# Optimization experiments

Hardware: AMD Instinct MI355X
Metric: run time of the kernel (lower is better)

Reference implementation:

```python
import jax, jax.numpy as jnp
import numpy as np

H = 16      # num_heads = num_channels // head_dim
D = 128     # head_dim
BLK = 64    # NABLA / flex_attention block size
THR = 0.8   # sparse_params['P'] cumulative-density threshold
EPS = 1e-6  # RMSNorm eps


def _rmsnorm(x, w):
    # torch nn.RMSNorm over last dim (computed in fp32 as in norm_qk)
    return x * jax.lax.rsqrt(jnp.mean(x * x, axis=-1, keepdims=True) + EPS) * w


def _rotate_half(x):
    x1, x2 = jnp.split(x, 2, axis=-1)
    return jnp.concatenate([-x2, x1], axis=-1)


def _apply_rotary(x, cos, sin):
    # x: [S, H, D]; cos/sin: [S, 1, D]
    return x * cos + _rotate_half(x) * sin


def _nabla_block_mask(q, k, sta_mask):
    # q, k: [H, S, D] -> block-pooled attention map, cumulative-density threshold
    Hh, S, Dd = q.shape
    nb = S // BLK
    qb = q.reshape(Hh, nb, BLK, Dd).mean(axis=2)           # [H, nQ, D]
    kb = k.reshape(Hh, nb, BLK, Dd).mean(axis=2)           # [H, nK, D]
    p = jax.nn.softmax(jnp.einsum('hqd,hkd->hqk', qb, kb) / np.sqrt(Dd), axis=-1)
    srt = -jnp.sort(-p, axis=-1)                           # descending
    csum = jnp.cumsum(srt, axis=-1)
    keep_sorted = (csum - srt) < THR                       # smallest set covering THR mass
    cutoff = jnp.min(jnp.where(keep_sorted, srt, jnp.inf), axis=-1, keepdims=True)
    return (p >= cutoff) | sta_mask[None]                  # [H, nQ, nK] bool


def reference(x, rope_cos, rope_sin, sta_mask, Wq, bq, Wk, bk, Wv, bv, Wo, bo, qn_w, kn_w):
    S, C = x.shape
    q = (x @ Wq + bq).reshape(S, H, D)
    k = (x @ Wk + bk).reshape(S, H, D)
    v = (x @ Wv + bv).reshape(S, H, D)
    q = _rmsnorm(q, qn_w)
    k = _rmsnorm(k, kn_w)
    q = _apply_rotary(q, rope_cos, rope_sin)
    k = _apply_rotary(k, rope_cos, rope_sin)
    q = q.transpose(1, 0, 2)  # [H, S, D]
    k = k.transpose(1, 0, 2)
    v = v.transpose(1, 0, 2)
    blk_keep = _nabla_block_mask(q, k, sta_mask)                     # [H, nQ, nK]
    mask = jnp.repeat(jnp.repeat(blk_keep, BLK, axis=1), BLK, axis=2)  # [H, S, S]
    scores = jnp.einsum('hqd,hkd->hqk', q, k) / np.sqrt(D)
    scores = jnp.where(mask, scores, -jnp.inf)
    attn = jax.nn.softmax(scores, axis=-1)
    out = jnp.einsum('hqk,hkd->hqd', attn, v)                        # [H, S, D]
    out = out.transpose(1, 0, 2).reshape(S, H * D)
    return out @ Wo + bo


def setup_inputs() -> dict:
    key = jax.random.key(0)
    ks = jax.random.split(key, 12)
    S, C = 2048, 2048
    nb = S // BLK
    sc = 0.02
    return {
        'x': jax.random.normal(ks[0], (S, C), jnp.float32),
        'rope_cos': jax.random.uniform(ks[1], (S, 1, D), jnp.float32),
        'rope_sin': jax.random.uniform(ks[2], (S, 1, D), jnp.float32),
        'sta_mask': jax.random.randint(ks[3], (nb, nb), 0, 2).astype(bool),
        'Wq': jax.random.normal(ks[4], (C, C), jnp.float32) * sc,
        'bq': jnp.zeros((C,), jnp.float32),
        'Wk': jax.random.normal(ks[5], (C, C), jnp.float32) * sc,
        'bk': jnp.zeros((C,), jnp.float32),
        'Wv': jax.random.normal(ks[6], (C, C), jnp.float32) * sc,
        'bv': jnp.zeros((C,), jnp.float32),
        'Wo': jax.random.normal(ks[7], (C, C), jnp.float32) * sc,
        'bo': jnp.zeros((C,), jnp.float32),
        'qn_w': jnp.ones((D,), jnp.float32),
        'kn_w': jnp.ones((D,), jnp.float32),
    }
```

## Files before the change

### kernel.cpp

```cpp
#include <hip/hip_runtime.h>


#define S_LEN 2048
#define CDIM  2048
#define NH    16
#define HD    128
#define NB    32

typedef __attribute__((ext_vector_type(8))) short s8v;
typedef __attribute__((ext_vector_type(4))) short s4v;
typedef __attribute__((ext_vector_type(4))) float f4v;

__device__ __forceinline__ short f2bf(float f){
  unsigned u = __builtin_bit_cast(unsigned, f);
  u += 0x7fffu + ((u>>16)&1u);
  return (short)(u>>16);
}
__device__ __forceinline__ float bf2f(short s){
  unsigned u = ((unsigned)(unsigned short)s)<<16;
  return __builtin_bit_cast(float, u);
}
__device__ __forceinline__ void gload_lds16(const void* g, void* l){
  __builtin_amdgcn_global_load_lds(
      (const __attribute__((address_space(1))) void*)g,
      (__attribute__((address_space(3))) void*)l, 16, 0, 0);
}

__global__ void __launch_bounds__(256) conv_x_kernel(
    const float* __restrict__ x, short* __restrict__ xcat)
{
  int i = blockIdx.x*256 + threadIdx.x;
  f4v v = ((const f4v*)x)[i];
  int s = i >> 9, c4 = (i & 511)*4;
  s4v hi, lo;
#pragma unroll
  for (int e=0;e<4;e++){
    short h = f2bf(v[e]);
    hi[e] = h;
    lo[e] = f2bf(v[e] - bf2f(h));
  }
  short* row = xcat + (size_t)s*4096 + c4;
  *(s4v*)(row)        = hi;
  *(s4v*)(row + 2048) = lo;
}

__global__ void __launch_bounds__(256) conv_w3_kernel(
    const float* __restrict__ Wq, const float* __restrict__ Wk,
    short* __restrict__ wcat)
{
  __shared__ float tile[64][65];
  const float* W = blockIdx.z ? Wk : Wq;
  short* out = wcat + (size_t)blockIdx.z*2048*4096;
  const int k0 = blockIdx.y*64, n0 = blockIdx.x*64, t = threadIdx.x;
#pragma unroll
  for (int i=0;i<16;i++){
    int idx = i*256 + t, r = idx>>6, c = idx&63;
    tile[r][c] = W[(size_t)(k0+r)*2048 + (n0+c)];
  }
  __syncthreads();
#pragma unroll
  for (int i=0;i<16;i++){
    int idx = i*256 + t, n = idx>>6, k = idx&63;
    float v = tile[k][n];
    short h  = f2bf(v);
    short lo = f2bf(v - bf2f(h));
    short* base = out + (size_t)(n0+n)*4096 + (k0+k);
    base[0]    = h;
    base[2048] = lo;
  }
}

__global__ void __launch_bounds__(256) conv_w1_kernel(
    const float* __restrict__ Wv, const float* __restrict__ Wo,
    short* __restrict__ wtv, short* __restrict__ wto)
{
  __shared__ float tile[64][65];
  const float* W = blockIdx.z ? Wo : Wv;
  short* wt = blockIdx.z ? wto : wtv;
  const int k0 = blockIdx.y*64, n0 = blockIdx.x*64, t = threadIdx.x;
#pragma unroll
  for (int i=0;i<16;i++){
    int idx = i*256 + t, r = idx>>6, c = idx&63;
    tile[r][c] = W[(size_t)(k0+r)*2048 + (n0+c)];
  }
  __syncthreads();
#pragma unroll
  for (int i=0;i<16;i++){
    int idx = i*256 + t, n = idx>>6, k = idx&63;
    wt[(size_t)(n0+n)*2048 + (k0+k)] = f2bf(tile[k][n]);
  }
}

template<int OUT>
__global__ void __launch_bounds__(512, 4) gemm8_bt(
    const short* __restrict__ A, int lda,
    const short* __restrict__ Bt, int ldb,
    const float* __restrict__ biasQ, const float* __restrict__ biasK,
    int nsplit,
    void* __restrict__ Cout, int ldc, int K, int ntiles,
    int awrap, int asub, int bwrap, int bsub)
{
  __shared__ short Alds[2][128*64];
  __shared__ short Blds[2][128*64];
  const int t = threadIdx.x, w = t>>6, l = t&63;
  const int nwg = gridDim.x;
  const int bid = blockIdx.x;
  const int swz = (bid & 7)*(nwg>>3) + (bid>>3);
  const int mi = swz / ntiles, ni = swz % ntiles;
  const int m0 = mi*128, n0 = ni*128;
  const int wr = w>>2, wc = w&3;
  const int l16 = l&15, lg = l>>4;

  f4v acc[4][2];
  f4v z = {0.f,0.f,0.f,0.f};
#pragma unroll
  for (int a=0;a<4;a++)
#pragma unroll
    for (int b=0;b<2;b++) acc[a][b] = z;

  const int srow = w*16 + (l>>3);
  const int scol = ((l&7) ^ ((l>>3)&7)) * 8;
  const short* Ag = A  + (size_t)(m0 + srow)*lda + scol;
  const short* Bg = Bt + (size_t)(n0 + srow)*ldb + scol;

  auto stageAB = [&](int buf, int kt){
    const int ak = kt - ((kt >= awrap) ? asub : 0);
    const int bk2 = kt - ((kt >= bwrap) ? bsub : 0);
#pragma unroll
    for (int ii=0;ii<2;ii++){
      gload_lds16(Ag + (size_t)ii*8*lda + ak, (char*)Alds[buf] + w*2048 + ii*1024);
      gload_lds16(Bg + (size_t)ii*8*ldb + bk2, (char*)Blds[buf] + w*2048 + ii*1024);
    }
  };

  stageAB(0, 0);
  int cur = 0;
  for (int kt = 0; kt < K; kt += 64){
    if (kt + 64 < K){
      stageAB(cur^1, kt+64);
      asm volatile("s_waitcnt vmcnt(4)" ::: "memory");
    } else {
      asm volatile("s_waitcnt vmcnt(0)" ::: "memory");
    }
    __builtin_amdgcn_s_barrier();
    const char* Al = (const char*)Alds[cur];
    const char* Bl = (const char*)Blds[cur];
#pragma unroll
    for (int kk=0;kk<2;kk++){
      const int swx = ((l16&7)<<4);
      s8v af[4], bfv[2];
#pragma unroll
      for (int mt=0;mt<4;mt++)
        af[mt]  = *(const s8v*)(Al + (wr*64+mt*16+l16)*128 + ((kk*64 + lg*16) ^ swx));
#pragma unroll
      for (int jt=0;jt<2;jt++)
        bfv[jt] = *(const s8v*)(Bl + (wc*32+jt*16+l16)*128 + ((kk*64 + lg*16) ^ swx));
      __builtin_amdgcn_s_setprio(1);
#pragma unroll
      for (int mt=0;mt<4;mt++)
#pragma unroll
        for (int jt=0;jt<2;jt++)
          acc[mt][jt] = __builtin_amdgcn_mfma_f32_16x16x32_bf16(
              af[mt], bfv[jt], acc[mt][jt], 0, 0, 0);
      __builtin_amdgcn_s_setprio(0);
    }
    asm volatile("" ::: "memory");
    __builtin_amdgcn_s_barrier();
    cur ^= 1;
  }

  const float* bp = (n0 >= nsplit) ? (biasK + (n0 - nsplit)) : (biasQ + n0);
#pragma unroll
  for (int mt=0;mt<4;mt++)
#pragma unroll
    for (int r=0;r<4;r++){
      int row = m0 + wr*64 + mt*16 + lg*4 + r;
#pragma unroll
      for (int jt=0;jt<2;jt++){
        int cr = wc*32 + jt*16 + l16;
        float v = acc[mt][jt][r] + bp[cr];
        if (OUT == 0) ((float*)Cout)[(size_t)row*ldc + n0 + cr] = v;
        else          ((short*)Cout)[(size_t)row*ldc + n0 + cr] = f2bf(v);
      }
    }
}

template<int OUT>
__global__ void __launch_bounds__(512, 6) gemm8_n64(
    const short* __restrict__ A, int lda,
    const short* __restrict__ Bt, int ldb,
    const float* __restrict__ bias,
    void* __restrict__ Cout, int ldc, int K, int ntiles)
{
  __shared__ short Alds[2][128*64];
  __shared__ short Blds[2][64*64];
  const int t = threadIdx.x, w = t>>6, l = t&63;
  const int nwg = gridDim.x;
  const int bid = blockIdx.x;
  const int swz = (bid & 7)*(nwg>>3) + (bid>>3);
  const int mi = swz / ntiles, ni = swz % ntiles;
  const int m0 = mi*128, n0 = ni*64;
  const int wr = w>>2, wc = w&3;
  const int l16 = l&15, lg = l>>4;

  f4v acc[4];
  f4v z = {0.f,0.f,0.f,0.f};
#pragma unroll
  for (int a=0;a<4;a++) acc[a] = z;

  const int srA = w*16 + (l>>3);
  const int srB = w*8  + (l>>3);
  const int scol = ((l&7) ^ ((l>>3)&7)) * 8;
  const short* Ag = A  + (size_t)(m0 + srA)*lda + scol;
  const short* Bg = Bt + (size_t)(n0 + srB)*ldb + scol;

  auto stageAB = [&](int buf, int kt){
#pragma unroll
    for (int ii=0;ii<2;ii++)
      gload_lds16(Ag + (size_t)ii*8*lda + kt, (char*)Alds[buf] + w*2048 + ii*1024);
    gload_lds16(Bg + kt, (char*)Blds[buf] + w*1024);
  };

  stageAB(0, 0);
  int cur = 0;
  for (int kt = 0; kt < K; kt += 64){
    if (kt + 64 < K){
      stageAB(cur^1, kt+64);
      asm volatile("s_waitcnt vmcnt(3)" ::: "memory");
    } else {
      asm volatile("s_waitcnt vmcnt(0)" ::: "memory");
    }
    __builtin_amdgcn_s_barrier();
    const char* Al = (const char*)Alds[cur];
    const char* Bl = (const char*)Blds[cur];
#pragma unroll
    for (int kk=0;kk<2;kk++){
      const int swx = ((l16&7)<<4);
      s8v af[4], bfv;
#pragma unroll
      for (int mt=0;mt<4;mt++)
        af[mt] = *(const s8v*)(Al + (wr*64+mt*16+l16)*128 + ((kk*64 + lg*16) ^ swx));
      bfv = *(const s8v*)(Bl + (wc*16+l16)*128 + ((kk*64 + lg*16) ^ swx));
      __builtin_amdgcn_s_setprio(1);
#pragma unroll
      for (int mt=0;mt<4;mt++)
        acc[mt] = __builtin_amdgcn_mfma_f32_16x16x32_bf16(af[mt], bfv, acc[mt], 0,0,0);
      __builtin_amdgcn_s_setprio(0);
    }
    asm volatile("" ::: "memory");
    __builtin_amdgcn_s_barrier();
    cur ^= 1;
  }

#pragma unroll
  for (int mt=0;mt<4;mt++)
#pragma unroll
    for (int r=0;r<4;r++){
      int row = m0 + wr*64 + mt*16 + lg*4 + r;
      int cr = wc*16 + l16;
      float v = acc[mt][r] + bias[n0 + cr];
      if (OUT == 0) ((float*)Cout)[(size_t)row*ldc + n0 + cr] = v;
      else          ((short*)Cout)[(size_t)row*ldc + n0 + cr] = f2bf(v);
    }
}

__global__ void __launch_bounds__(256) qk_post_kernel(
    const float* __restrict__ QKf,
    const float* __restrict__ qw, const float* __restrict__ kw,
    const float* __restrict__ rc, const float* __restrict__ rs,
    short* __restrict__ Qh, short* __restrict__ Kh,
    float* __restrict__ Qb, float* __restrict__ Kb)
{
  __shared__ float pool[4][128];
  const int sb = blockIdx.x, h = blockIdx.y, which = blockIdx.z;
  const float* in    = QKf + (which ? 2048 : 0);
  const float* wvp   = which ? kw : qw;
  short*       outp  = which ? Kh : Qh;
  float*       poolp = which ? Kb : Qb;
  const int t = threadIdx.x, w = t>>6, l = t&63;
  const int s = sb*64 + w*16 + (l>>2), d0 = (l&3)*32;

  float a[32];
  const f4v* src = (const f4v*)(in + (size_t)s*4096 + h*128 + d0);
#pragma unroll
  for (int i=0;i<8;i++){
    f4v v = src[i];
    a[i*4]=v[0]; a[i*4+1]=v[1]; a[i*4+2]=v[2]; a[i*4+3]=v[3];
  }
  float ss = 0.f;
#pragma unroll
  for (int i=0;i<32;i++) ss += a[i]*a[i];
  ss += __shfl_xor(ss,1); ss += __shfl_xor(ss,2);
  float rstd = 1.0f / sqrtf(ss*(1.0f/128.0f) + 1e-6f);

  const f4v* wv4 = (const f4v*)(wvp + d0);
#pragma unroll
  for (int i=0;i<8;i++){
    f4v wv = wv4[i];
    a[i*4]   *= rstd*wv[0]; a[i*4+1] *= rstd*wv[1];
    a[i*4+2] *= rstd*wv[2]; a[i*4+3] *= rstd*wv[3];
  }
  float cv[32], sv[32];
  const f4v* cs4 = (const f4v*)(rc + (size_t)s*128 + d0);
  const f4v* sn4 = (const f4v*)(rs + (size_t)s*128 + d0);
#pragma unroll
  for (int i=0;i<8;i++){
    f4v c = cs4[i], sn = sn4[i];
    cv[i*4]=c[0]; cv[i*4+1]=c[1]; cv[i*4+2]=c[2]; cv[i*4+3]=c[3];
    sv[i*4]=sn[0]; sv[i*4+1]=sn[1]; sv[i*4+2]=sn[2]; sv[i*4+3]=sn[3];
  }
  const float sgn = (l&2) ? 1.f : -1.f;
#pragma unroll
  for (int i=0;i<32;i++){
    float pv = __shfl_xor(a[i], 2);
    a[i] = a[i]*cv[i] + sgn*pv*sv[i];
  }
  short* op = outp + ((size_t)h*2048 + s)*128 + d0;
#pragma unroll
  for (int c8=0;c8<8;c8++){
    s4v ob;
#pragma unroll
    for (int e=0;e<4;e++) ob[e] = f2bf(a[c8*4+e]);
    ((s4v*)op)[c8] = ob;
  }
#pragma unroll
  for (int i=0;i<32;i++){
    a[i] += __shfl_xor(a[i],4);
    a[i] += __shfl_xor(a[i],8);
    a[i] += __shfl_xor(a[i],16);
    a[i] += __shfl_xor(a[i],32);
  }
  if ((l>>2)==0){
#pragma unroll
    for (int i=0;i<32;i++) pool[w][d0+i] = a[i];
  }
  __syncthreads();
  if (t < 128)
    poolp[((size_t)h*32 + sb)*128 + t] =
        (pool[0][t]+pool[1][t]+pool[2][t]+pool[3][t]) * (1.0f/64.0f);
}

__global__ void __launch_bounds__(64) nabla_mask_kernel(
    const float* __restrict__ Qb, const float* __restrict__ Kb,
    const void* __restrict__ sta, unsigned char* __restrict__ keep)
{
  const int qi = blockIdx.x, h = blockIdx.y, l = threadIdx.x;
  const int j = l & 31;
  const int* si = (const int*)sta;
  int wv0 = si[j];
  int isInt = __all((wv0==0) | (wv0==1));

  const f4v* qr = (const f4v*)(Qb + ((size_t)h*32+qi)*128);
  const f4v* kr = (const f4v*)(Kb + ((size_t)h*32+j)*128);
  float dot = 0.f;
#pragma unroll
  for (int d=0; d<32; d++){
    f4v a = qr[d], b = kr[d];
    dot += a[0]*b[0] + a[1]*b[1] + a[2]*b[2] + a[3]*b[3];
  }
  float logit = dot / sqrtf(128.0f);
  float mx = logit;
  mx = fmaxf(mx, __shfl_xor(mx,1));  mx = fmaxf(mx, __shfl_xor(mx,2));
  mx = fmaxf(mx, __shfl_xor(mx,4));  mx = fmaxf(mx, __shfl_xor(mx,8));
  mx = fmaxf(mx, __shfl_xor(mx,16));
  float e = expf(logit - mx);
  float den = e;
  den += __shfl_xor(den,1);  den += __shfl_xor(den,2);
  den += __shfl_xor(den,4);  den += __shfl_xor(den,8);
  den += __shfl_xor(den,16);
  float p = e / den;
  float Sg = 0.f;
  for (int jj=0;jj<32;jj++){
    float pj = __shfl(p, jj);
    if (pj > p) Sg += pj;
  }
  float cand = (Sg < 0.8f) ? p : 3.0e38f;
  float cut = cand;
  cut = fminf(cut, __shfl_xor(cut,1));  cut = fminf(cut, __shfl_xor(cut,2));
  cut = fminf(cut, __shfl_xor(cut,4));  cut = fminf(cut, __shfl_xor(cut,8));
  cut = fminf(cut, __shfl_xor(cut,16));
  bool stab = isInt ? (si[qi*32+j] != 0)
                    : (((const unsigned char*)sta)[qi*32+j] != 0);
  if (l < 32)
    keep[((size_t)(h*32)+qi)*32 + j] = ((p >= cut) || stab) ? 1 : 0;
}

__global__ void __launch_bounds__(256) v_trans_kernel(
    const short* __restrict__ v_sd, short* __restrict__ vt)
{
  __shared__ short tile[64][65];
  const int sb = blockIdx.x, db = blockIdx.y, h = blockIdx.z, t = threadIdx.x;
#pragma unroll
  for (int i=0;i<16;i++){
    int idx = i*256 + t, r = idx>>6, c = idx&63;
    tile[r][c] = v_sd[(size_t)(sb*64+r)*2048 + h*128 + db*64 + c];
  }
  __syncthreads();
#pragma unroll
  for (int i=0;i<16;i++){
    int idx = i*256 + t, dn = idx>>6, s2 = idx&63;
    vt[((size_t)h*128 + db*64 + dn)*2048 + sb*64 + s2] = tile[s2][dn];
  }
}

__global__ void __launch_bounds__(256) attn_fwd_kernel(
    const short* __restrict__ qh, const short* __restrict__ kh,
    const short* __restrict__ vt, const unsigned char* __restrict__ keep,
    short* __restrict__ attn_out)
{
  __shared__ short Klds[2][64*128];
  __shared__ short Vlds[2][128*64];
  __shared__ short Plds[4][1024];
  const int bid = blockIdx.x;
  const int swz = (bid & 7)*64 + (bid >> 3);
  const int h = swz >> 5, qb = swz & 31;
  const int t = threadIdx.x, w = t>>6, l = t&63;
  const int l16 = l&15, lg = l>>4;

  s8v qf[4];
  const int sq0 = qb*64 + w*16;
  const short* qbase = qh + ((size_t)h*2048 + sq0 + l16)*128 + lg*8;
#pragma unroll
  for (int kf=0;kf<4;kf++) qf[kf] = *(const s8v*)(qbase + kf*32);

  f4v acc[8];
  f4v z = {0.f,0.f,0.f,0.f};
#pragma unroll
  for (int d=0;d<8;d++) acc[d] = z;
  float mrow[4], lsum[4];
#pragma unroll
  for (int r=0;r<4;r++){ mrow[r] = -3.0e38f; lsum[r] = 0.f; }

  const unsigned char* keeprow = keep + ((size_t)(h*32) + qb)*32;
  const short* kg0 = kh + (size_t)h*2048*128;
  const short* vg0 = vt + (size_t)h*128*2048;

  unsigned km = 0;
#pragma unroll
  for (int j=0;j<32;j++) km |= ((unsigned)keeprow[j]) << j;
  if (!km) km = 1;

  auto stageKV = [&](int buf, int j){
    const char* kg = (const char*)(kg0 + (size_t)(j*64)*128);
    const char* vg = (const char*)(vg0 + j*64);
#pragma unroll
    for (int ii=0;ii<4;ii++){
      int kr = (w*4+ii)*4 + (l>>4);
      int ks = ((l&15)*16) ^ ((kr&7)<<4);
      gload_lds16(kg + (size_t)kr*256 + ks, (char*)Klds[buf] + (w*4+ii)*1024);
      int vr = (w*4+ii)*8 + (l>>3);
      int vs = ((l&7)*16) ^ ((vr&7)<<4);
      gload_lds16(vg + (size_t)vr*4096 + vs, (char*)Vlds[buf] + (w*4+ii)*1024);
    }
  };

  asm volatile("s_waitcnt vmcnt(0)" ::: "memory");
  int jcur = (int)__builtin_ctz(km); km &= km-1;
  stageKV(0, jcur);
  int cur = 0;

  while (jcur >= 0){
    int jn = -1;
    if (km){ jn = (int)__builtin_ctz(km); km &= km-1; }
    if (jn >= 0){
      stageKV(cur^1, jn);
      asm volatile("s_waitcnt vmcnt(8)" ::: "memory");
    } else {
      asm volatile("s_waitcnt vmcnt(0)" ::: "memory");
    }
    __builtin_amdgcn_s_barrier();

    const char* Kl = (const char*)Klds[cur];
    const char* Vl = (const char*)Vlds[cur];

    f4v sacc[4];
#pragma unroll
    for (int nt=0;nt<4;nt++) sacc[nt] = z;
    __builtin_amdgcn_s_setprio(1);
#pragma unroll
    for (int kf=0;kf<4;kf++)
#pragma unroll
      for (int nt=0;nt<4;nt++){
        int kr = nt*16 + l16;
        s8v bfr = *(const s8v*)(Kl + ((kr*256 + kf*64 + lg*16) ^ ((kr&7)<<4)));
        sacc[nt] = __builtin_amdgcn_mfma_f32_16x16x32_bf16(qf[kf], bfr, sacc[nt], 0,0,0);
      }
    __builtin_amdgcn_s_setprio(0);
    const float scl = 0.08838834764831845f;
#pragma unroll
    for (int nt=0;nt<4;nt++) sacc[nt] *= scl;

#pragma unroll
    for (int r=0;r<4;r++){
      float mx = fmaxf(fmaxf(sacc[0][r], sacc[1][r]),
                       fmaxf(sacc[2][r], sacc[3][r]));
      mx = fmaxf(mx, __shfl_xor(mx,1));  mx = fmaxf(mx, __shfl_xor(mx,2));
      mx = fmaxf(mx, __shfl_xor(mx,4));  mx = fmaxf(mx, __shfl_xor(mx,8));
      if (mx > mrow[r]){
        float resc = __expf(mrow[r] - mx);
        mrow[r] = mx;
        lsum[r] *= resc;
#pragma unroll
        for (int dt=0;dt<8;dt++) acc[dt][r] *= resc;
      }
      float psum = 0.f;
#pragma unroll
      for (int nt=0;nt<4;nt++){
        float p = __expf(sacc[nt][r] - mrow[r]);
        sacc[nt][r] = p;
        psum += p;
      }
      psum += __shfl_xor(psum,1);  psum += __shfl_xor(psum,2);
      psum += __shfl_xor(psum,4);  psum += __shfl_xor(psum,8);
      lsum[r] += psum;
    }

    char* Pl = (char*)Plds[w];
#pragma unroll
    for (int nt=0;nt<4;nt++)
#pragma unroll
      for (int r=0;r<4;r++){
        int pr = lg*4 + r;
        *(short*)(Pl + ((pr*128 + nt*32 + l16*2) ^ ((pr&7)<<4))) = f2bf(sacc[nt][r]);
      }
    s8v pa0 = *(const s8v*)(Pl + ((l16*128 +  0 + lg*16) ^ ((l16&7)<<4)));
    s8v pa1 = *(const s8v*)(Pl + ((l16*128 + 64 + lg*16) ^ ((l16&7)<<4)));

    __builtin_amdgcn_s_setprio(1);
#pragma unroll
    for (int kk=0;kk<2;kk++){
      s8v pa = kk ? pa1 : pa0;
#pragma unroll
      for (int dt=0;dt<8;dt++){
        int vr = dt*16 + l16;
        s8v vb = *(const s8v*)(Vl + ((vr*128 + kk*64 + lg*16) ^ ((vr&7)<<4)));
        acc[dt] = __builtin_amdgcn_mfma_f32_16x16x32_bf16(pa, vb, acc[dt], 0,0,0);
      }
    }
    __builtin_amdgcn_s_setprio(0);

    asm volatile("" ::: "memory");
    __builtin_amdgcn_s_barrier();
    cur ^= 1; jcur = jn;
  }

#pragma unroll
  for (int r=0;r<4;r++){
    float inv = 1.0f / lsum[r];
    int s = qb*64 + w*16 + lg*4 + r;
#pragma unroll
    for (int dt=0;dt<8;dt++)
      attn_out[(size_t)s*2048 + h*128 + dt*16 + l16] = f2bf(acc[dt][r]*inv);
  }
}

extern "C" void kernel_launch(void* const* d_in, const int* in_sizes, int n_in,
                              void* d_out, int out_size, void* d_ws, size_t ws_size,
                              hipStream_t stream)
{
  (void)in_sizes; (void)n_in; (void)out_size; (void)ws_size;
  const float* x   = (const float*)d_in[0];
  const float* rc  = (const float*)d_in[1];
  const float* rs  = (const float*)d_in[2];
  const void*  sta = d_in[3];
  const float* Wq  = (const float*)d_in[4];
  const float* bq  = (const float*)d_in[5];
  const float* Wk  = (const float*)d_in[6];
  const float* bk  = (const float*)d_in[7];
  const float* Wv  = (const float*)d_in[8];
  const float* bv  = (const float*)d_in[9];
  const float* Wo  = (const float*)d_in[10];
  const float* bo  = (const float*)d_in[11];
  const float* qnw = (const float*)d_in[12];
  const float* knw = (const float*)d_in[13];

  char* ws = (char*)d_ws;
  size_t off = 0;
  auto take = [&](size_t b){ char* p = ws + off; off = (off + b + 255) & ~(size_t)255; return p; };
  short* Xcat  = (short*)take((size_t)2048*4096*2);
  short* Wcat2 = (short*)take((size_t)4096*4096*2);
  short* Wt1v  = (short*)take((size_t)2048*2048*2);
  short* Wt1o  = (short*)take((size_t)2048*2048*2);
  float* QKf   = (float*)take((size_t)2048*4096*4);
  short* Vsd   = (short*)take((size_t)2048*2048*2);
  short* Qh    = (short*)take((size_t)NH*2048*128*2);
  short* Kh    = (short*)take((size_t)NH*2048*128*2);
  float* Qb    = (float*)take((size_t)NH*32*128*4);
  float* Kb    = (float*)take((size_t)NH*32*128*4);
  unsigned char* Keep = (unsigned char*)take(NH*32*32);
  short* AttnO = (short*)QKf;
  short* Vt    = (short*)((char*)QKf + (size_t)16*1024*1024);

  conv_x_kernel <<<4096, 256, 0, stream>>>(x, Xcat);
  conv_w3_kernel<<<dim3(32,32,2), 256, 0, stream>>>(Wq, Wk, Wcat2);
  gemm8_bt<0><<<512, 512, 0, stream>>>(Xcat, 4096, Wcat2, 4096, bq, bk, 2048,
                                       QKf, 4096, 6144, 32,
                                       2048, 2048, 4096, 4096);
  conv_w1_kernel<<<dim3(32,32,2), 256, 0, stream>>>(Wv, Wo, Wt1v, Wt1o);
  gemm8_n64<1><<<512, 512, 0, stream>>>(Xcat, 4096, Wt1v, 2048, bv,
                                        Vsd, 2048, 2048, 32);
  qk_post_kernel<<<dim3(32,16,2), 256, 0, stream>>>(QKf, qnw, knw, rc, rs, Qh, Kh, Qb, Kb);
  v_trans_kernel<<<dim3(32,2,16), 256, 0, stream>>>(Vsd, Vt);
  nabla_mask_kernel<<<dim3(32,16), 64, 0, stream>>>(Qb, Kb, sta, Keep);
  attn_fwd_kernel<<<512, 256, 0, stream>>>(Qh, Kh, Vt, Keep, AttnO);
  gemm8_n64<0><<<512, 512, 0, stream>>>((const short*)AttnO, 2048, Wt1o, 2048, bo,
                                        d_out, 2048, 2048, 32);
}
```

Measured before the change: 513.2 us.

## Split attention KV blocks across two workgroups and merge partials in combine kernel

Each query tile's kept KV blocks are split alternately between two workgroups, doubling the attention grid from 512 to 1024 blocks. Each writes unnormalized fp32 accumulators plus row max and sum to scratch, and a new combine kernel merges them with log-sum-exp rescaling and writes the bf16 output. The online softmax update becomes branchless so it also handles partitions with no blocks. This targets underutilization of the GPU's compute units at 512 workgroups, at the cost of extra fp32 traffic, an extra launch and unconditional rescaling.

```diff
diff --git a/kernel.cpp b/kernel.cpp
--- a/kernel.cpp
+++ b/kernel.cpp
@@ -406,13 +406,15 @@
 __global__ void __launch_bounds__(256) attn_fwd_kernel(
     const short* __restrict__ qh, const short* __restrict__ kh,
     const short* __restrict__ vt, const unsigned char* __restrict__ keep,
-    short* __restrict__ attn_out)
+    float* __restrict__ accP, float* __restrict__ mlP)
 {
   __shared__ short Klds[2][64*128];
   __shared__ short Vlds[2][128*64];
   __shared__ short Plds[4][1024];
   const int bid = blockIdx.x;
-  const int swz = (bid & 7)*64 + (bid >> 3);
+  const int part = bid >> 9;
+  const int inner = bid & 511;
+  const int swz = (inner & 7)*64 + (inner >> 3);
   const int h = swz >> 5, qb = swz & 31;
   const int t = threadIdx.x, w = t>>6, l = t&63;
   const int l16 = l&15, lg = l>>4;
@@ -439,6 +441,14 @@
 #pragma unroll
   for (int j=0;j<32;j++) km |= ((unsigned)keeprow[j]) << j;
   if (!km) km = 1;
+
+  unsigned kmp = 0; int idx = 0;
+  for (int j=0;j<32;j++){
+    if ((km>>j)&1u){
+      if ((idx & 1) == part) kmp |= (1u<<j);
+      idx++;
+    }
+  }
 
   auto stageKV = [&](int buf, int j){
     const char* kg = (const char*)(kg0 + (size_t)(j*64)*128);
@@ -455,13 +465,13 @@
   };
 
   asm volatile("s_waitcnt vmcnt(0)" ::: "memory");
-  int jcur = (int)__builtin_ctz(km); km &= km-1;
-  stageKV(0, jcur);
+  int jcur = -1;
+  if (kmp){ jcur = (int)__builtin_ctz(kmp); kmp &= kmp-1; stageKV(0, jcur); }
   int cur = 0;
 
   while (jcur >= 0){
     int jn = -1;
-    if (km){ jn = (int)__builtin_ctz(km); km &= km-1; }
+    if (kmp){ jn = (int)__builtin_ctz(kmp); kmp &= kmp-1; }
     if (jn >= 0){
       stageKV(cur^1, jn);
       asm volatile("s_waitcnt vmcnt(8)" ::: "memory");
@@ -496,23 +506,21 @@
                        fmaxf(sacc[2][r], sacc[3][r]));
       mx = fmaxf(mx, __shfl_xor(mx,1));  mx = fmaxf(mx, __shfl_xor(mx,2));
       mx = fmaxf(mx, __shfl_xor(mx,4));  mx = fmaxf(mx, __shfl_xor(mx,8));
-      if (mx > mrow[r]){
-        float resc = __expf(mrow[r] - mx);
-        mrow[r] = mx;
-        lsum[r] *= resc;
-#pragma unroll
-        for (int dt=0;dt<8;dt++) acc[dt][r] *= resc;
-      }
+      float mnew = fmaxf(mrow[r], mx);
+      float resc = __expf(mrow[r] - mnew);
+      mrow[r] = mnew;
       float psum = 0.f;
 #pragma unroll
       for (int nt=0;nt<4;nt++){
-        float p = __expf(sacc[nt][r] - mrow[r]);
+        float p = __expf(sacc[nt][r] - mnew);
         sacc[nt][r] = p;
         psum += p;
       }
       psum += __shfl_xor(psum,1);  psum += __shfl_xor(psum,2);
       psum += __shfl_xor(psum,4);  psum += __shfl_xor(psum,8);
-      lsum[r] += psum;
+      lsum[r] = lsum[r]*resc + psum;
+#pragma unroll
+      for (int dt=0;dt<8;dt++) acc[dt][r] *= resc;
     }
 
     char* Pl = (char*)Plds[w];
@@ -544,14 +552,40 @@
     cur ^= 1; jcur = jn;
   }
 
+  const int pb = part*512 + h*32 + qb;
+  float* accp = accP + (size_t)pb*8192;
+  float* mlp  = mlP  + (size_t)pb*128;
 #pragma unroll
   for (int r=0;r<4;r++){
-    float inv = 1.0f / lsum[r];
-    int s = qb*64 + w*16 + lg*4 + r;
+    int row = w*16 + lg*4 + r;
+    if (l16 == 0){ mlp[row] = mrow[r]; mlp[64 + row] = lsum[r]; }
 #pragma unroll
     for (int dt=0;dt<8;dt++)
-      attn_out[(size_t)s*2048 + h*128 + dt*16 + l16] = f2bf(acc[dt][r]*inv);
-  }
+      accp[row*128 + dt*16 + l16] = acc[dt][r];
+  }
+}
+
+__global__ void __launch_bounds__(256) combine_kernel(
+    const float* __restrict__ accP, const float* __restrict__ mlP,
+    short* __restrict__ out)
+{
+  int gid = blockIdx.x*256 + threadIdx.x;
+  int dq  = (gid & 31) * 4;
+  int rowg = gid >> 5;
+  int h = rowg >> 11, s = rowg & 2047;
+  int qb = s >> 6, r = s & 63;
+  int pb0 = h*32 + qb, pb1 = pb0 + 512;
+  float m0 = mlP[pb0*128 + r], l0 = mlP[pb0*128 + 64 + r];
+  float m1 = mlP[pb1*128 + r], l1 = mlP[pb1*128 + 64 + r];
+  float m = fmaxf(m0, m1);
+  float a0 = __expf(m0 - m), a1 = __expf(m1 - m);
+  float inv = 1.0f / (l0*a0 + l1*a1);
+  f4v v0 = *(const f4v*)(accP + (size_t)pb0*8192 + r*128 + dq);
+  f4v v1 = *(const f4v*)(accP + (size_t)pb1*8192 + r*128 + dq);
+  s4v ob;
+#pragma unroll
+  for (int e=0;e<4;e++) ob[e] = f2bf((v0[e]*a0 + v1[e]*a1) * inv);
+  *(s4v*)(out + (size_t)s*2048 + h*128 + dq) = ob;
 }
 
 extern "C" void kernel_launch(void* const* d_in, const int* in_sizes, int n_in,
@@ -590,6 +624,8 @@
   unsigned char* Keep = (unsigned char*)take(NH*32*32);
   short* AttnO = (short*)QKf;
   short* Vt    = (short*)((char*)QKf + (size_t)16*1024*1024);
+  float* accP  = (float*)Wcat2;
+  float* mlP   = (float*)Wt1v;
 
   conv_x_kernel <<<4096, 256, 0, stream>>>(x, Xcat);
   conv_w3_kernel<<<dim3(32,32,2), 256, 0, stream>>>(Wq, Wk, Wcat2);
@@ -602,7 +638,8 @@
   qk_post_kernel<<<dim3(32,16,2), 256, 0, stream>>>(QKf, qnw, knw, rc, rs, Qh, Kh, Qb, Kb);
   v_trans_kernel<<<dim3(32,2,16), 256, 0, stream>>>(Vsd, Vt);
   nabla_mask_kernel<<<dim3(32,16), 64, 0, stream>>>(Qb, Kb, sta, Keep);
-  attn_fwd_kernel<<<512, 256, 0, stream>>>(Qh, Kh, Vt, Keep, AttnO);
+  attn_fwd_kernel<<<1024, 256, 0, stream>>>(Qh, Kh, Vt, Keep, accP, mlP);
+  combine_kernel<<<4096, 256, 0, stream>>>(accP, mlP, AttnO);
   gemm8_n64<0><<<512, 512, 0, stream>>>((const short*)AttnO, 2048, Wt1o, 2048, bo,
                                         d_out, 2048, 2048, 32);
 }
```

Result: faster. 447.2 us (-12.9%).
